# Optimization experiments

Hardware: AMD Instinct MI355X
Metric: run time of the kernel (lower is better)

Reference implementation:

```python
import jax, jax.numpy as jnp
import numpy as np

NUM_CLASSES = 5  # sleep stages: W, N1, N2, N3, REM
N = 4194304


def setup_inputs() -> dict:
    key = jax.random.key(0)
    k1, k2 = jax.random.split(key)
    inputs = jax.random.normal(k1, (N, NUM_CLASSES), dtype=jnp.float32)
    targets = jax.random.randint(k2, (N,), 0, NUM_CLASSES, dtype=jnp.int32)
    return {"inputs": inputs, "targets": targets}


def reference(inputs, targets):
    # Mean False Error loss: per-class mean of per-sample cross-entropy,
    # summed over classes that are present in the batch.
    # per-sample CE loss (stable log-softmax, single pass)
    logp = jax.nn.log_softmax(inputs, axis=-1)                    # [N, C]
    per_sample = -jnp.take_along_axis(logp, targets[:, None].astype(jnp.int32), axis=1)[:, 0]  # [N]
    # segment-reduce by class label (replaces the python grouping loop)
    loss_sums = jax.ops.segment_sum(per_sample, targets, num_segments=NUM_CLASSES)             # [C]
    counts = jax.ops.segment_sum(jnp.ones_like(per_sample), targets, num_segments=NUM_CLASSES) # [C]
    # per-class mean; empty classes contribute 0
    means = jnp.where(counts > 0, loss_sums / jnp.maximum(counts, 1.0), 0.0)
    return jnp.sum(means)
```

## Files before the change

### kernel.cpp

```cpp
#include <hip/hip_runtime.h>

#define NCLS 5
#define NSAMP 4194304
#define BLOCK 256
#define GRID 2048
#define NTHREADS (GRID * BLOCK)
#define ITERS (NSAMP / (NTHREADS * 4))
#define NVALS (2 * NCLS)

__device__ __forceinline__ void accum_sample(float l0, float l1, float l2, float l3, float l4,
                                             int t, float sums[NCLS], unsigned int& packed_cnt) {
    float s = __expf(l0) + __expf(l1) + __expf(l2) + __expf(l3) + __expf(l4);
    float lt = (t == 0) ? l0 : (t == 1) ? l1 : (t == 2) ? l2 : (t == 3) ? l3 : l4;
    float ce = __logf(s) - lt;
#pragma unroll
    for (int k = 0; k < NCLS; ++k) {
        sums[k] += (t == k) ? ce : 0.0f;
    }
    packed_cnt += 1u << (6 * t);
}

__device__ __forceinline__ void block_reduce_10(float sums[NCLS], float cnts[NCLS],
                                                float* result10) {
#pragma unroll
    for (int k = 0; k < NCLS; ++k) {
#pragma unroll
        for (int off = 32; off > 0; off >>= 1) {
            sums[k] += __shfl_down(sums[k], off, 64);
            cnts[k] += __shfl_down(cnts[k], off, 64);
        }
    }
    __shared__ float ls[BLOCK / 64][NVALS];
    const int lane = threadIdx.x & 63;
    const int wave = threadIdx.x >> 6;
    if (lane == 0) {
#pragma unroll
        for (int k = 0; k < NCLS; ++k) {
            ls[wave][k] = sums[k];
            ls[wave][NCLS + k] = cnts[k];
        }
    }
    __syncthreads();
    if (threadIdx.x < NVALS) {
        float v = 0.f;
#pragma unroll
        for (int w = 0; w < BLOCK / 64; ++w) v += ls[w][threadIdx.x];
        *result10 = v;
    }
}

__global__ __launch_bounds__(BLOCK) void mfe_partial(const float* __restrict__ inputs,
                                                     const int* __restrict__ targets,
                                                     float* __restrict__ partial ) {
    const int tid = blockIdx.x * BLOCK + threadIdx.x;

    const int base0 = tid * 4;
    const int base1 = (NTHREADS + tid) * 4;
    const float4* p0 = (const float4*)(inputs + (size_t)base0 * NCLS);
    const float4* p1 = (const float4*)(inputs + (size_t)base1 * NCLS);
    float4 a0 = p0[0], b0 = p0[1], c0 = p0[2], d0 = p0[3], e0 = p0[4];
    float4 a1 = p1[0], b1 = p1[1], c1 = p1[2], d1 = p1[3], e1 = p1[4];
    int4 t0 = *(const int4*)(targets + base0);
    int4 t1 = *(const int4*)(targets + base1);

    float sums[NCLS] = {0.f, 0.f, 0.f, 0.f, 0.f};
    unsigned int packed = 0;

    accum_sample(a0.x, a0.y, a0.z, a0.w, b0.x, t0.x, sums, packed);
    accum_sample(b0.y, b0.z, b0.w, c0.x, c0.y, t0.y, sums, packed);
    accum_sample(c0.z, c0.w, d0.x, d0.y, d0.z, t0.z, sums, packed);
    accum_sample(d0.w, e0.x, e0.y, e0.z, e0.w, t0.w, sums, packed);
    accum_sample(a1.x, a1.y, a1.z, a1.w, b1.x, t1.x, sums, packed);
    accum_sample(b1.y, b1.z, b1.w, c1.x, c1.y, t1.y, sums, packed);
    accum_sample(c1.z, c1.w, d1.x, d1.y, d1.z, t1.z, sums, packed);
    accum_sample(d1.w, e1.x, e1.y, e1.z, e1.w, t1.w, sums, packed);

    float cnts[NCLS];
#pragma unroll
    for (int k = 0; k < NCLS; ++k) {
        cnts[k] = (float)((packed >> (6 * k)) & 63u);
    }

    float total;
    block_reduce_10(sums, cnts, &total);
    if (threadIdx.x < NVALS) {
        partial[threadIdx.x * GRID + blockIdx.x] = total;
    }
}

__global__ __launch_bounds__(BLOCK) void mfe_final(const float* __restrict__ partial,
                                                   float* __restrict__ out) {
    float sums[NCLS];
    float cnts[NCLS];
#pragma unroll
    for (int k = 0; k < NCLS; ++k) {
        float s = 0.f, c = 0.f;
#pragma unroll
        for (int i = 0; i < GRID / BLOCK; ++i) {
            s += partial[k * GRID + threadIdx.x + i * BLOCK];
            c += partial[(NCLS + k) * GRID + threadIdx.x + i * BLOCK];
        }
        sums[k] = s;
        cnts[k] = c;
    }

    float total;
    block_reduce_10(sums, cnts, &total);

    __shared__ float fin[NVALS];
    if (threadIdx.x < NVALS) fin[threadIdx.x] = total;
    __syncthreads();
    if (threadIdx.x == 0) {
        float loss = 0.f;
#pragma unroll
        for (int k = 0; k < NCLS; ++k) {
            float cnt = fin[NCLS + k];
            if (cnt > 0.f) loss += fin[k] / cnt;
        }
        out[0] = loss;
    }
}

extern "C" void kernel_launch(void* const* d_in, const int* in_sizes, int n_in,
                              void* d_out, int out_size, void* d_ws, size_t ws_size,
                              hipStream_t stream) {
    const float* inputs = (const float*)d_in[0];
    const int* targets = (const int*)d_in[1];
    float* out = (float*)d_out;
    float* partial = (float*)d_ws;

    mfe_partial<<<GRID, BLOCK, 0, stream>>>(inputs, targets, partial);
    mfe_final<<<1, BLOCK, 0, stream>>>(partial, out);
}
```

Before: 135.8 us.

## Stage input rows through LDS with global_load_lds for coalesced wave chunks

Replaces per-thread strided float4 loads of 5-float rows with per-wave contiguous 1280-float chunks copied into LDS via the direct global-to-LDS load builtin. Each lane then reads its 20 floats from LDS. The intent is fully coalesced global reads that bypass VGPRs for the staging. The cost is explicit waitcnt serialization per chunk with no double buffering, plus extra LDS traffic and possible bank conflicts from the stride-20 LDS reads. The block reduction is inlined and reuses the staging buffer.

New measurement: 137.1 us. No clear change (+1.0%).

```diff
diff --git a/kernel.cpp b/kernel.cpp
--- a/kernel.cpp
+++ b/kernel.cpp
@@ -4,9 +4,18 @@
 #define NSAMP 4194304
 #define BLOCK 256
 #define GRID 2048
-#define NTHREADS (GRID * BLOCK)
-#define ITERS (NSAMP / (NTHREADS * 4))
+#define WAVES (BLOCK / 64)
 #define NVALS (2 * NCLS)
+#define WCHUNKS (NSAMP / 256)
+#define CPW (WCHUNKS / (GRID * WAVES))
+#define CHUNK_F 1280
+
+__device__ __forceinline__ void stage16(const float* gsrc, float* ldst) {
+    __builtin_amdgcn_global_load_lds(
+        (const __attribute__((address_space(1))) void*)gsrc,
+        (__attribute__((address_space(3))) void*)ldst,
+        16, 0, 0);
+}
 
 __device__ __forceinline__ void accum_sample(float l0, float l1, float l2, float l3, float l4,
                                              int t, float sums[NCLS], unsigned int& packed_cnt) {
@@ -20,8 +29,91 @@
     packed_cnt += 1u << (6 * t);
 }
 
-__device__ __forceinline__ void block_reduce_10(float sums[NCLS], float cnts[NCLS],
-                                                float* result10) {
+__global__ __launch_bounds__(BLOCK) void mfe_partial(const float* __restrict__ inputs,
+                                                     const int* __restrict__ targets,
+                                                     float* __restrict__ partial ) {
+    __shared__ float lds_buf[WAVES * CHUNK_F];
+    const int lane = threadIdx.x & 63;
+    const int wave = threadIdx.x >> 6;
+    float* wbuf = lds_buf + wave * CHUNK_F;
+
+    float sums[NCLS] = {0.f, 0.f, 0.f, 0.f, 0.f};
+    unsigned int packed = 0;
+
+#pragma unroll
+    for (int c = 0; c < CPW; ++c) {
+        const int g = (c * GRID + (int)blockIdx.x) * WAVES + wave;
+        const float* gsrc = inputs + (size_t)g * CHUNK_F;
+
+        __builtin_amdgcn_s_waitcnt(0xC07F);
+#pragma unroll
+        for (int j = 0; j < 5; ++j)
+            stage16(gsrc + j * 256 + lane * 4, wbuf + j * 256);
+        int4 t4 = *(const int4*)(targets + (size_t)g * 256 + lane * 4);
+
+        __builtin_amdgcn_s_waitcnt(0x0F70);
+
+        const float* sp = wbuf + lane * 20;
+        float4 a = *(const float4*)(sp + 0);
+        float4 b = *(const float4*)(sp + 4);
+        float4 cc = *(const float4*)(sp + 8);
+        float4 d = *(const float4*)(sp + 12);
+        float4 e = *(const float4*)(sp + 16);
+
+        accum_sample(a.x, a.y, a.z, a.w, b.x, t4.x, sums, packed);
+        accum_sample(b.y, b.z, b.w, cc.x, cc.y, t4.y, sums, packed);
+        accum_sample(cc.z, cc.w, d.x, d.y, d.z, t4.z, sums, packed);
+        accum_sample(d.w, e.x, e.y, e.z, e.w, t4.w, sums, packed);
+    }
+
+    float cnts[NCLS];
+#pragma unroll
+    for (int k = 0; k < NCLS; ++k) {
+        cnts[k] = (float)((packed >> (6 * k)) & 63u);
+    }
+
+#pragma unroll
+    for (int k = 0; k < NCLS; ++k) {
+#pragma unroll
+        for (int off = 32; off > 0; off >>= 1) {
+            sums[k] += __shfl_down(sums[k], off, 64);
+            cnts[k] += __shfl_down(cnts[k], off, 64);
+        }
+    }
+
+    __syncthreads();
+    if (lane == 0) {
+#pragma unroll
+        for (int k = 0; k < NCLS; ++k) {
+            lds_buf[wave * NVALS + k] = sums[k];
+            lds_buf[wave * NVALS + NCLS + k] = cnts[k];
+        }
+    }
+    __syncthreads();
+    if (threadIdx.x < NVALS) {
+        float v = 0.f;
+#pragma unroll
+        for (int w = 0; w < WAVES; ++w) v += lds_buf[w * NVALS + threadIdx.x];
+        partial[threadIdx.x * GRID + blockIdx.x] = v;
+    }
+}
+
+__global__ __launch_bounds__(BLOCK) void mfe_final(const float* __restrict__ partial,
+                                                   float* __restrict__ out) {
+    float sums[NCLS];
+    float cnts[NCLS];
+#pragma unroll
+    for (int k = 0; k < NCLS; ++k) {
+        float s = 0.f, c = 0.f;
+#pragma unroll
+        for (int i = 0; i < GRID / BLOCK; ++i) {
+            s += partial[k * GRID + threadIdx.x + i * BLOCK];
+            c += partial[(NCLS + k) * GRID + threadIdx.x + i * BLOCK];
+        }
+        sums[k] = s;
+        cnts[k] = c;
+    }
+
 #pragma unroll
     for (int k = 0; k < NCLS; ++k) {
 #pragma unroll
@@ -41,74 +133,14 @@
         }
     }
     __syncthreads();
+
+    __shared__ float fin[NVALS];
     if (threadIdx.x < NVALS) {
         float v = 0.f;
 #pragma unroll
         for (int w = 0; w < BLOCK / 64; ++w) v += ls[w][threadIdx.x];
-        *result10 = v;
+        fin[threadIdx.x] = v;
     }
-}
-
-__global__ __launch_bounds__(BLOCK) void mfe_partial(const float* __restrict__ inputs,
-                                                     const int* __restrict__ targets,
-                                                     float* __restrict__ partial ) {
-    const int tid = blockIdx.x * BLOCK + threadIdx.x;
-
-    const int base0 = tid * 4;
-    const int base1 = (NTHREADS + tid) * 4;
-    const float4* p0 = (const float4*)(inputs + (size_t)base0 * NCLS);
-    const float4* p1 = (const float4*)(inputs + (size_t)base1 * NCLS);
-    float4 a0 = p0[0], b0 = p0[1], c0 = p0[2], d0 = p0[3], e0 = p0[4];
-    float4 a1 = p1[0], b1 = p1[1], c1 = p1[2], d1 = p1[3], e1 = p1[4];
-    int4 t0 = *(const int4*)(targets + base0);
-    int4 t1 = *(const int4*)(targets + base1);
-
-    float sums[NCLS] = {0.f, 0.f, 0.f, 0.f, 0.f};
-    unsigned int packed = 0;
-
-    accum_sample(a0.x, a0.y, a0.z, a0.w, b0.x, t0.x, sums, packed);
-    accum_sample(b0.y, b0.z, b0.w, c0.x, c0.y, t0.y, sums, packed);
-    accum_sample(c0.z, c0.w, d0.x, d0.y, d0.z, t0.z, sums, packed);
-    accum_sample(d0.w, e0.x, e0.y, e0.z, e0.w, t0.w, sums, packed);
-    accum_sample(a1.x, a1.y, a1.z, a1.w, b1.x, t1.x, sums, packed);
-    accum_sample(b1.y, b1.z, b1.w, c1.x, c1.y, t1.y, sums, packed);
-    accum_sample(c1.z, c1.w, d1.x, d1.y, d1.z, t1.z, sums, packed);
-    accum_sample(d1.w, e1.x, e1.y, e1.z, e1.w, t1.w, sums, packed);
-
-    float cnts[NCLS];
-#pragma unroll
-    for (int k = 0; k < NCLS; ++k) {
-        cnts[k] = (float)((packed >> (6 * k)) & 63u);
-    }
-
-    float total;
-    block_reduce_10(sums, cnts, &total);
-    if (threadIdx.x < NVALS) {
-        partial[threadIdx.x * GRID + blockIdx.x] = total;
-    }
-}
-
-__global__ __launch_bounds__(BLOCK) void mfe_final(const float* __restrict__ partial,
-                                                   float* __restrict__ out) {
-    float sums[NCLS];
-    float cnts[NCLS];
-#pragma unroll
-    for (int k = 0; k < NCLS; ++k) {
-        float s = 0.f, c = 0.f;
-#pragma unroll
-        for (int i = 0; i < GRID / BLOCK; ++i) {
-            s += partial[k * GRID + threadIdx.x + i * BLOCK];
-            c += partial[(NCLS + k) * GRID + threadIdx.x + i * BLOCK];
-        }
-        sums[k] = s;
-        cnts[k] = c;
-    }
-
-    float total;
-    block_reduce_10(sums, cnts, &total);
-
-    __shared__ float fin[NVALS];
-    if (threadIdx.x < NVALS) fin[threadIdx.x] = total;
     __syncthreads();
     if (threadIdx.x == 0) {
         float loss = 0.f;
```
